# Kernel optimization log

Measured on AMD Instinct MI355X. Metric: run time of the kernel, lower is better.

The kernel has to match this reference:

```python
import jax, jax.numpy as jnp
import numpy as np

B, L = 4, 2048
D_MODEL = 64          # d_model = input_size
ED = 128              # d_inner = expand_factor * d_model = hidden_size
N = 32                # d_state
DCONV = 16            # d_conv
NLAYERS = 4
DTRANK = 4            # ceil(d_model/16)
NCLS = 1
EPS = 1e-5


def setup_inputs() -> dict:
    key = jax.random.key(0)
    ks = jax.random.split(key, 10)
    g = lambda k, s, sc: jax.random.normal(k, s, dtype=jnp.float32) * sc
    inp = {}
    inp["x"] = jax.random.normal(ks[0], (B, L, D_MODEL), dtype=jnp.float32)
    inp["in_w"] = g(ks[1], (NLAYERS, 2 * ED, D_MODEL), 0.1)
    inp["in_b"] = jnp.zeros((NLAYERS, 2 * ED), jnp.float32)
    inp["conv_w"] = g(ks[2], (NLAYERS, ED, 1, DCONV), 0.1)  # depthwise kernel (OIH per group)
    inp["conv_b"] = jnp.zeros((NLAYERS, ED), jnp.float32)
    inp["xproj_w"] = g(ks[3], (NLAYERS, DTRANK + 2 * N, ED), 0.1)
    inp["dtproj_w"] = g(ks[4], (NLAYERS, ED, DTRANK), 0.5)
    inp["dtproj_b"] = g(ks[5], (NLAYERS, ED), 0.5)
    # S4D-real init: A[e, n] = n+1
    A = jnp.tile(jnp.arange(1, N + 1, dtype=jnp.float32), (ED, 1))
    inp["A_log"] = jnp.tile(jnp.log(A)[None], (NLAYERS, 1, 1))
    inp["Dp"] = jnp.ones((NLAYERS, ED), jnp.float32)
    inp["outproj_w"] = g(ks[6], (NLAYERS, D_MODEL, ED), 0.1)
    inp["outproj_b"] = jnp.zeros((NLAYERS, D_MODEL), jnp.float32)
    inp["norm_w"] = jnp.ones((NLAYERS, D_MODEL), jnp.float32)
    inp["fc_w"] = g(ks[7], (NCLS, ED), 0.1)
    inp["fc_b"] = jnp.zeros((NCLS,), jnp.float32)
    return inp


def _rmsnorm(x, w):
    return x * jax.lax.rsqrt(jnp.mean(x * x, axis=-1, keepdims=True) + EPS) * w


def _causal_dwconv(x, w, b):
    # x: [B,L,ED], w: [ED,1,DCONV] depthwise, causal left pad
    xt = jnp.swapaxes(x, 1, 2)  # [B,ED,L]
    y = jax.lax.conv_general_dilated(
        xt, w, window_strides=(1,), padding=[(DCONV - 1, 0)],
        dimension_numbers=("NCH", "OIH", "NCH"), feature_group_count=ED)
    return jnp.swapaxes(y, 1, 2) + b


def _mamba_block(h, in_w, in_b, conv_w, conv_b, xproj_w, dtproj_w, dtproj_b,
                 A_log, Dp, outproj_w, outproj_b, last):
    xz = jnp.einsum("bld,ed->ble", h, in_w) + in_b          # [B,L,2ED]
    xin, z = jnp.split(xz, 2, axis=-1)
    xc = jax.nn.silu(_causal_dwconv(xin, conv_w, conv_b))    # [B,L,ED]
    dbc = jnp.einsum("ble,re->blr", xc, xproj_w)             # [B,L,DTRANK+2N]
    delta = dbc[..., :DTRANK]
    Bm = dbc[..., DTRANK:DTRANK + N]                          # [B,L,N]
    Cm = dbc[..., DTRANK + N:]                                # [B,L,N]
    delta = jax.nn.softplus(jnp.einsum("blr,er->ble", delta, dtproj_w) + dtproj_b)
    A = -jnp.exp(A_log)                                       # [ED,N]
    dA = jnp.exp(delta[..., None] * A)                        # [B,L,ED,N]
    dBu = delta[..., None] * Bm[:, :, None, :] * xc[..., None]  # [B,L,ED,N]

    def step(hs, t):
        dA_t, dBu_t, C_t = t                                  # [B,ED,N],[B,ED,N],[B,N]
        hs = dA_t * hs + dBu_t
        y = jnp.einsum("ben,bn->be", hs, C_t)
        return hs, y

    h0 = jnp.zeros((xc.shape[0], ED, N), dtype=xc.dtype)
    _, ys = jax.lax.scan(step, h0, (jnp.swapaxes(dA, 0, 1),
                                    jnp.swapaxes(dBu, 0, 1),
                                    jnp.swapaxes(Cm, 0, 1)))
    y = jnp.swapaxes(ys, 0, 1) + Dp * xc                      # [B,L,ED]
    y = y * jax.nn.silu(z)
    if last:
        return y                                              # classifier taps d_inner features
    return jnp.einsum("ble,de->bld", y, outproj_w) + outproj_b


def reference(x, in_w, in_b, conv_w, conv_b, xproj_w, dtproj_w, dtproj_b,
              A_log, Dp, outproj_w, outproj_b, norm_w, fc_w, fc_b):
    h = x
    for i in range(NLAYERS - 1):
        h = h + _mamba_block(_rmsnorm(h, norm_w[i]), in_w[i], in_b[i], conv_w[i],
                             conv_b[i], xproj_w[i], dtproj_w[i], dtproj_b[i],
                             A_log[i], Dp[i], outproj_w[i], outproj_b[i], False)
    i = NLAYERS - 1
    y = _mamba_block(_rmsnorm(h, norm_w[i]), in_w[i], in_b[i], conv_w[i],
                     conv_b[i], xproj_w[i], dtproj_w[i], dtproj_b[i],
                     A_log[i], Dp[i], outproj_w[i], outproj_b[i], True)
    last_hidden = y[:, -1, :]                                 # [B,ED]
    return last_hidden @ fc_w.T + fc_b                        # [B,NCLS]
```

## Files before the change

kernel.cpp:

```cpp
#include <hip/hip_runtime.h>
#include <math.h>

#define BSZ 4
#define Lseq 2048
#define DM 64
#define ED 128
#define NST 32
#define DCONVK 16
#define NLAYERS 4
#define DTRANK 4
#define EPSV 1e-5f
#define NC 128
#define TT 16
#define NSEG 8
#define GRIDN (BSZ * NC)
#define L2E 1.4426950408889634f

#if defined(__has_builtin)
#if __has_builtin(__builtin_amdgcn_exp2f)
#define EXP2F(x) __builtin_amdgcn_exp2f(x)
#else
#define EXP2F(x) exp2f(x)
#endif
#else
#define EXP2F(x) exp2f(x)
#endif

__device__ __forceinline__ float sigf(float x) { return 1.0f / (1.0f + __expf(-x)); }
__device__ __forceinline__ float hsum4(float4 a) { return (a.x + a.y) + (a.z + a.w); }

__device__ __forceinline__ float ldsc(const float* p) {
    return __hip_atomic_load((float*)p, __ATOMIC_RELAXED, __HIP_MEMORY_SCOPE_AGENT);
}
__device__ __forceinline__ void stsc(float* p, float v) {
    __hip_atomic_store(p, v, __ATOMIC_RELAXED, __HIP_MEMORY_SCOPE_AGENT);
}
__device__ __forceinline__ unsigned long long ldsc64(const void* p) {
    return __hip_atomic_load((unsigned long long*)p, __ATOMIC_RELAXED,
                             __HIP_MEMORY_SCOPE_AGENT);
}
__device__ __forceinline__ void stsc64(void* p, unsigned long long v) {
    __hip_atomic_store((unsigned long long*)p, v, __ATOMIC_RELAXED,
                       __HIP_MEMORY_SCOPE_AGENT);
}

__device__ __forceinline__ void gbar(unsigned int* cnt, unsigned int* rel,
                                     unsigned int k)
{
    __syncthreads();
    if (blockIdx.x == 0) {
        if (threadIdx.x == 0) {
            __hip_atomic_fetch_add(cnt, 1u, __ATOMIC_RELAXED, __HIP_MEMORY_SCOPE_AGENT);
            while (__hip_atomic_load(cnt, __ATOMIC_RELAXED, __HIP_MEMORY_SCOPE_AGENT)
                   < k * (unsigned)GRIDN)
                __builtin_amdgcn_s_sleep(1);
        }
        __syncthreads();
        __hip_atomic_store(&rel[threadIdx.x * 16], k,
                           __ATOMIC_RELAXED, __HIP_MEMORY_SCOPE_AGENT);
        __hip_atomic_store(&rel[(threadIdx.x + 256) * 16], k,
                           __ATOMIC_RELAXED, __HIP_MEMORY_SCOPE_AGENT);
    } else {
        if (threadIdx.x == 0) {
            __hip_atomic_fetch_add(cnt, 1u, __ATOMIC_RELAXED, __HIP_MEMORY_SCOPE_AGENT);
            while (__hip_atomic_load(&rel[blockIdx.x * 16], __ATOMIC_RELAXED,
                                     __HIP_MEMORY_SCOPE_AGENT) < k)
                __builtin_amdgcn_s_sleep(2);
        }
    }
    __builtin_amdgcn_sched_barrier(0);
    __syncthreads();
}

__device__ __forceinline__ void inproj16(
    const float* in_w_l, const float* in_b_l, const float (*hn)[DM],
    float* xin, float* zbuf, size_t t0, int tid)
{
    float4 w4[16];
    const float4* wr = (const float4*)(in_w_l + tid * DM);
    #pragma unroll
    for (int i = 0; i < 16; ++i) w4[i] = wr[i];
    const float bias = in_b_l[tid];
    #pragma unroll 2
    for (int tok = 0; tok < TT; ++tok) {
        const float4* hv4 = (const float4*)&hn[tok][0];
        float4 a4 = make_float4(0.f, 0.f, 0.f, 0.f);
        #pragma unroll
        for (int i = 0; i < 16; ++i) {
            float4 hv = hv4[i];
            a4.x = fmaf(hv.x, w4[i].x, a4.x);
            a4.y = fmaf(hv.y, w4[i].y, a4.y);
            a4.z = fmaf(hv.z, w4[i].z, a4.z);
            a4.w = fmaf(hv.w, w4[i].w, a4.w);
        }
        const float r = bias + hsum4(a4);
        if (tid < ED) stsc(&xin[(t0 + tok) * ED + tid], r);
        else          stsc(&zbuf[(t0 + tok) * ED + (tid - ED)], r);
    }
}

struct KParams {
    const float *x, *in_w, *in_b, *conv_w, *conv_b, *xproj_w, *dtproj_w,
                *dtproj_b, *A_log, *Dp, *outproj_w, *outproj_b, *norm_w,
                *fc_w, *fc_b;
    float *out, *h0, *h1, *xin, *zbuf, *xc, *dlt, *Bv, *Cv, *dsum, *hloc;
    unsigned int *cnt, *rel;
};

__global__ __launch_bounds__(256, 2) void k_mamba(KParams P)
{
    const int bid = blockIdx.x;
    const int tid = threadIdx.x;
    unsigned int bk = 0;
    __shared__ __align__(16) float smem[12288];

    if (bid == 0 && tid < BSZ) stsc(&P.out[tid], 0.f);

    {
        float (*hn)[DM] = (float (*)[DM])smem;
        const size_t t0 = (size_t)bid * TT;
        const int lane = tid & 63, wv = tid >> 6;
        const float nw = P.norm_w[lane];
        float hval[4];
        #pragma unroll
        for (int j = 0; j < 4; ++j)
            hval[j] = P.x[(t0 + wv * 4 + j) * DM + lane];
        #pragma unroll
        for (int j = 0; j < 4; ++j) {
            float ss = hval[j] * hval[j];
            #pragma unroll
            for (int off = 32; off; off >>= 1) ss += __shfl_xor(ss, off, 64);
            const float sc = rsqrtf(ss * (1.0f / DM) + EPSV);
            hn[wv * 4 + j][lane] = hval[j] * sc * nw;
        }
        __syncthreads();
        inproj16(P.in_w, P.in_b, (const float (*)[DM])hn, P.xin, P.zbuf, t0, tid);
    }
    gbar(P.cnt, P.rel, ++bk);

    #pragma unroll 1
    for (int li = 0; li < NLAYERS; ++li) {
        const int last = (li == NLAYERS - 1);
        const float* Alog = P.A_log + (size_t)li * ED * NST;
        const float* Dpl  = P.Dp + (size_t)li * ED;

        {
            const int b = bid >> 7, c = bid & 127;
            const int l0 = c * TT;
            const size_t t0 = (size_t)b * Lseq + l0;
            const int e = tid & 127, half = tid >> 7;
            const int store_dbc = last ? 0 : 1;
            const bool doXC = store_dbc || (c == NC - 1);

            float* xs = smem;
            float (*xcs)[ED] = (float (*)[ED])(smem + 4096);
            float (*Bs)[NST] = (float (*)[NST])(smem + 6144);
            float (*dts)[DTRANK] = (float (*)[DTRANK])(smem + 6656);
            float* hsT = smem + 6720;
            float (*dl)[ED] = (float (*)[ED])xs;

            const float* conv_w   = P.conv_w + (size_t)li * ED * DCONVK;
            const float* conv_b   = P.conv_b + (size_t)li * ED;
            const float* xproj_w  = P.xproj_w + (size_t)li * (DTRANK + 2 * NST) * ED;
            const float* dtproj_w = P.dtproj_w + (size_t)li * ED * DTRANK;
            const float* dtproj_b = P.dtproj_b + (size_t)li * ED;

            float Aen16[16];
            {
                const float4* a4 = (const float4*)(Alog + e * NST + half * 16);
                #pragma unroll
                for (int i = 0; i < 4; ++i) {
                    float4 v = a4[i];
                    Aen16[i*4+0] = -__expf(v.x) * L2E; Aen16[i*4+1] = -__expf(v.y) * L2E;
                    Aen16[i*4+2] = -__expf(v.z) * L2E; Aen16[i*4+3] = -__expf(v.w) * L2E;
                }
            }
            float w[DCONVK];
            {
                const float4* cw = (const float4*)(conv_w + e * DCONVK);
                #pragma unroll
                for (int i = 0; i < 4; ++i) {
                    float4 cc = cw[i];
                    w[i*4+0] = cc.x; w[i*4+1] = cc.y; w[i*4+2] = cc.z; w[i*4+3] = cc.w;
                }
            }
            const float cb = conv_b[e];

            {
                float hv[8];
                #pragma unroll
                for (int i = 0; i < 8; ++i) {
                    const int idx = tid + i * 256;
                    float val = 0.f;
                    if (idx < (DCONVK - 1) * ED) {
                        const int row = idx >> 7;
                        const int col = idx & 127;
                        const int lrow = l0 - (DCONVK - 1) + row;
                        if (lrow >= 0)
                            val = ldsc(P.xin + ((size_t)b * Lseq + lrow) * ED + col);
                    }
                    hv[i] = val;
                }
                float4 ov[2];
                #pragma unroll
                for (int i = 0; i < 2; ++i) {
                    const int idx4 = 480 + tid + i * 256;
                    const int row = idx4 >> 5;
                    const int lrow = l0 - (DCONVK - 1) + row;
                    ov[i] = ((const float4*)(P.xin + ((size_t)b * Lseq + lrow) * ED))[idx4 & 31];
                }
                #pragma unroll
                for (int i = 0; i < 8; ++i) {
                    const int idx = tid + i * 256;
                    if (idx < (DCONVK - 1) * ED) xs[idx] = hv[i];
                }
                #pragma unroll
                for (int i = 0; i < 2; ++i)
                    ((float4*)xs)[480 + tid + i * 256] = ov[i];
            }
            __syncthreads();

            {
                #pragma unroll 2
                for (int j = 0; j < 8; ++j) {
                    const int tok = half * 8 + j;
                    float acc = cb;
                    #pragma unroll
                    for (int k = 0; k < DCONVK; ++k)
                        acc = fmaf(xs[(tok + k) * ED + e], w[k], acc);
                    const float xcv = acc * sigf(acc);
                    xcs[tok][e] = xcv;
                    if (doXC) {
                        if (store_dbc) P.xc[(t0 + tok) * ED + e] = xcv;
                        else           stsc(&P.xc[(t0 + tok) * ED + e], xcv);
                    }
                }
            }
            __syncthreads();

            {
                const int wv = tid >> 6, lane = tid & 63;
                float4 acc[4];
                #pragma unroll
                for (int j = 0; j < 4; ++j) acc[j] = make_float4(0.f, 0.f, 0.f, 0.f);
                #pragma unroll 1
                for (int p = 0; p < 4; ++p) {
                    float4 w4[8];
                    const float4* wr = (const float4*)(xproj_w + lane * ED + p * 32);
                    #pragma unroll
                    for (int i = 0; i < 8; ++i) w4[i] = wr[i];
                    #pragma unroll
                    for (int j = 0; j < 4; ++j) {
                        const float4* yv = (const float4*)&xcs[wv * 4 + j][p * 32];
                        #pragma unroll
                        for (int i = 0; i < 8; ++i) {
                            float4 hv = yv[i];
                            acc[j].x = fmaf(hv.x, w4[i].x, acc[j].x);
                            acc[j].y = fmaf(hv.y, w4[i].y, acc[j].y);
                            acc[j].z = fmaf(hv.z, w4[i].z, acc[j].z);
                            acc[j].w = fmaf(hv.w, w4[i].w, acc[j].w);
                        }
                    }
                }
                #pragma unroll
                for (int j = 0; j < 4; ++j) {
                    const int tok = wv * 4 + j;
                    const float v = hsum4(acc[j]);
                    if (lane < DTRANK) {
                        dts[tok][lane] = v;
                    } else if (lane < DTRANK + NST) {
                        Bs[tok][lane - DTRANK] = v;
                        if (store_dbc) P.Bv[(t0 + tok) * NST + (lane - DTRANK)] = v;
                    } else {
                        if (doXC) {
                            const int ci = lane - DTRANK - NST;
                            if (store_dbc) P.Cv[(t0 + tok) * NST + ci] = v;
                            else           stsc(&P.Cv[(t0 + tok) * NST + ci], v);
                        }
                    }
                }
                {
                    const int ridx = lane & 3;
                    const int ks   = (lane >> 2) & 3;
                    const int tsub = lane >> 4;
                    const int r4   = 64 + ridx;
                    const int tok  = wv * 4 + tsub;
                    const float4* wr = (const float4*)(xproj_w + r4 * ED + ks * 32);
                    const float4* yv = (const float4*)&xcs[tok][ks * 32];
                    float4 a4 = make_float4(0.f, 0.f, 0.f, 0.f);
                    #pragma unroll
                    for (int i = 0; i < 8; ++i) {
                        float4 hv = yv[i]; float4 wv4 = wr[i];
                        a4.x = fmaf(hv.x, wv4.x, a4.x);
                        a4.y = fmaf(hv.y, wv4.y, a4.y);
                        a4.z = fmaf(hv.z, wv4.z, a4.z);
                        a4.w = fmaf(hv.w, wv4.w, a4.w);
                    }
                    float v = hsum4(a4);
                    v += __shfl_xor(v, 4, 64);
                    v += __shfl_xor(v, 8, 64);
                    if (ks == 0 && doXC) {
                        const int ci = r4 - DTRANK - NST;
                        if (store_dbc) P.Cv[(t0 + tok) * NST + ci] = v;
                        else           stsc(&P.Cv[(t0 + tok) * NST + ci], v);
                    }
                }
            }
            __syncthreads();

            {
                const float4 dwv = *(const float4*)(dtproj_w + e * DTRANK);
                const float bias = dtproj_b[e];
                #pragma unroll 2
                for (int j = 0; j < 8; ++j) {
                    const int tok = half * 8 + j;
                    float a = bias;
                    a = fmaf(dts[tok][0], dwv.x, a);
                    a = fmaf(dts[tok][1], dwv.y, a);
                    a = fmaf(dts[tok][2], dwv.z, a);
                    a = fmaf(dts[tok][3], dwv.w, a);
                    const float sp = fmaxf(a, 0.f) + log1pf(__expf(-fabsf(a)));
                    dl[tok][e] = sp;
                    if (store_dbc) P.dlt[(t0 + tok) * ED + e] = sp;
                }
            }
            __syncthreads();

            {
                float dsum = 0.f;
                #pragma unroll 4
                for (int l = 0; l < TT; ++l) dsum += dl[l][e];
                if (half == 0) stsc(&P.dsum[((size_t)b * NC + c) * ED + e], dsum);

                #pragma unroll 1
                for (int g = 0; g < 2; ++g) {
                    const int n0 = half * 16 + g * 8;
                    float Aen[8];
                    #pragma unroll
                    for (int k = 0; k < 8; ++k) Aen[k] = Aen16[g * 8 + k];
                    float hs[8];
                    #pragma unroll
                    for (int k = 0; k < 8; ++k) hs[k] = 0.f;
                    #pragma unroll 2
                    for (int l = 0; l < TT; ++l) {
                        const float de   = dl[l][e];
                        const float dexc = de * xcs[l][e];
                        const float4 B0 = *(const float4*)&Bs[l][n0];
                        const float4 B1 = *(const float4*)&Bs[l][n0 + 4];
                        float a;
                        a = EXP2F(de * Aen[0]); hs[0] = fmaf(a, hs[0], B0.x * dexc);
                        a = EXP2F(de * Aen[1]); hs[1] = fmaf(a, hs[1], B0.y * dexc);
                        a = EXP2F(de * Aen[2]); hs[2] = fmaf(a, hs[2], B0.z * dexc);
                        a = EXP2F(de * Aen[3]); hs[3] = fmaf(a, hs[3], B0.w * dexc);
                        a = EXP2F(de * Aen[4]); hs[4] = fmaf(a, hs[4], B1.x * dexc);
                        a = EXP2F(de * Aen[5]); hs[5] = fmaf(a, hs[5], B1.y * dexc);
                        a = EXP2F(de * Aen[6]); hs[6] = fmaf(a, hs[6], B1.z * dexc);
                        a = EXP2F(de * Aen[7]); hs[7] = fmaf(a, hs[7], B1.w * dexc);
                    }
                    #pragma unroll
                    for (int k = 0; k < 8; ++k) hsT[e * 33 + n0 + k] = hs[k];
                }
                __syncthreads();
                {
                    unsigned long long* dst =
                        (unsigned long long*)(P.hloc + (size_t)bid * (ED * NST));
                    #pragma unroll
                    for (int it = 0; it < 8; ++it) {
                        const int idx = tid + it * 256;
                        const int ee = idx >> 4;
                        const int nn = (idx & 15) * 2;
                        union { float f[2]; unsigned long long u; } pk;
                        pk.f[0] = hsT[ee * 33 + nn];
                        pk.f[1] = hsT[ee * 33 + nn + 1];
                        stsc64(dst + idx, pk.u);
                    }
                }
            }
        }
        gbar(P.cnt, P.rel, ++bk);

        {
            const int tt  = tid & 31;
            const int seg = tid >> 5;
            const int t   = bid * 32 + tt;
            const int b   = t >> 12;
            const int en  = t & 4095;
            const int e   = en >> 5;

            const float Aen2 = -__expf(Alog[en]) * L2E;

            const int c0 = seg * (NC / NSEG);
            const size_t idxBase = (size_t)b * NC * (ED * NST) + en;
            const size_t dBase   = (size_t)b * NC * ED + e;

            float u[NC / NSEG], a[NC / NSEG];
            #pragma unroll
            for (int k = 0; k < NC / NSEG; ++k)
                u[k] = ldsc(P.hloc + idxBase + (size_t)(c0 + k) * (ED * NST));
            #pragma unroll
            for (int k = 0; k < NC / NSEG; ++k)
                a[k] = EXP2F(Aen2 * ldsc(P.dsum + dBase + (size_t)(c0 + k) * ED));

            float A = 1.f, U = 0.f;
            #pragma unroll
            for (int k = 0; k < NC / NSEG; ++k) { U = fmaf(a[k], U, u[k]); A *= a[k]; }

            float (*As)[32] = (float (*)[32])smem;
            float (*Us)[32] = (float (*)[32])(smem + NSEG * 32);
            As[seg][tt] = A; Us[seg][tt] = U;
            __syncthreads();

            float h = 0.f;
            #pragma unroll
            for (int j = 0; j < NSEG - 1; ++j)
                if (j < seg) h = fmaf(As[j][tt], h, Us[j][tt]);

            #pragma unroll
            for (int k = 0; k < NC / NSEG; ++k) {
                stsc(P.hloc + idxBase + (size_t)(c0 + k) * (ED * NST), h);
                h = fmaf(a[k], h, u[k]);
            }

            if (last && seg == NSEG - 1) {
                const int n = en & 31;
                const size_t tok = (size_t)b * Lseq + (Lseq - 1);
                float p = h * ldsc(P.Cv + tok * NST + n);
                #pragma unroll
                for (int off = 16; off; off >>= 1) p += __shfl_xor(p, off, 32);
                if (n == 0) {
                    const float xce = ldsc(P.xc + tok * ED + e);
                    const float zi  = ldsc(P.zbuf + tok * ED + e);
                    float val = (p + Dpl[e] * xce) * (zi * sigf(zi)) * P.fc_w[e];
                    if (en == 0) val += P.fc_b[0];
                    atomicAdd(&P.out[b], val);
                }
            }
        }

        if (!last) {
            gbar(P.cnt, P.rel, ++bk);
            {
                const int b = bid >> 7, c = bid & 127;
                const int l0 = c * TT;
                const size_t t0 = (size_t)b * Lseq + l0;
                const int e = tid & 127, half = tid >> 7;

                float (*dlS)[ED] = (float (*)[ED])(smem);
                float (*xcS)[ED] = (float (*)[ED])(smem + 2048);
                float (*BsS)[NST] = (float (*)[NST])(smem + 4096);
                float (*CsS)[NST] = (float (*)[NST])(smem + 4608);
                float (*ys)[ED]  = (float (*)[ED])(smem + 5120);
                float (*pp)[TT][ED] = (float (*)[TT][ED])(smem + 7168);
                float (*hn)[DM]  = (float (*)[DM])(smem + 11264);

                const float* ow = P.outproj_w + (size_t)li * DM * ED;
                const float* ob = P.outproj_b + (size_t)li * DM;
                const float* hres = (li == 0) ? P.x : ((li == 1) ? P.h0 : P.h1);
                float* hout = (li & 1) ? P.h1 : P.h0;

                float Aen16[16];
                {
                    const float4* a4 = (const float4*)(Alog + e * NST + half * 16);
                    #pragma unroll
                    for (int i = 0; i < 4; ++i) {
                        float4 v = a4[i];
                        Aen16[i*4+0] = -__expf(v.x) * L2E; Aen16[i*4+1] = -__expf(v.y) * L2E;
                        Aen16[i*4+2] = -__expf(v.z) * L2E; Aen16[i*4+3] = -__expf(v.w) * L2E;
                    }
                }

                {
                    const float4* dsrc = (const float4*)(P.dlt + t0 * ED);
                    const float4* xsrc = (const float4*)(P.xc + t0 * ED);
                    float4* ddst = (float4*)&dlS[0][0];
                    float4* xdst = (float4*)&xcS[0][0];
                    #pragma unroll
                    for (int i = 0; i < 2; ++i) {
                        ddst[tid + i * 256] = dsrc[tid + i * 256];
                        xdst[tid + i * 256] = xsrc[tid + i * 256];
                    }
                    if (tid < 128) {
                        ((float4*)&BsS[0][0])[tid] = ((const float4*)(P.Bv + t0 * NST))[tid];
                        ((float4*)&CsS[0][0])[tid] = ((const float4*)(P.Cv + t0 * NST))[tid];
                    }
                }
                __syncthreads();

                #pragma unroll 1
                for (int g = 0; g < 2; ++g) {
                    const int n0 = half * 16 + g * 8;
                    float Aen[8];
                    #pragma unroll
                    for (int k = 0; k < 8; ++k) Aen[k] = Aen16[g * 8 + k];
                    float hs[8];
                    {
                        const size_t idx = (((size_t)b * NC + c) * ED + e) * NST + n0;
                        const unsigned long long* src =
                            (const unsigned long long*)(P.hloc + idx);
                        #pragma unroll
                        for (int k = 0; k < 4; ++k) {
                            union { float f[2]; unsigned long long u; } pk;
                            pk.u = ldsc64(src + k);
                            hs[2 * k]     = pk.f[0];
                            hs[2 * k + 1] = pk.f[1];
                        }
                    }
                    #pragma unroll 2
                    for (int l = 0; l < TT; ++l) {
                        const float de   = dlS[l][e];
                        const float dexc = de * xcS[l][e];
                        const float4 B0 = *(const float4*)&BsS[l][n0];
                        const float4 B1 = *(const float4*)&BsS[l][n0 + 4];
                        const float4 C0 = *(const float4*)&CsS[l][n0];
                        const float4 C1 = *(const float4*)&CsS[l][n0 + 4];
                        float a, p = 0.f;
                        a = EXP2F(de * Aen[0]); hs[0] = fmaf(a, hs[0], B0.x * dexc); p = fmaf(hs[0], C0.x, p);
                        a = EXP2F(de * Aen[1]); hs[1] = fmaf(a, hs[1], B0.y * dexc); p = fmaf(hs[1], C0.y, p);
                        a = EXP2F(de * Aen[2]); hs[2] = fmaf(a, hs[2], B0.z * dexc); p = fmaf(hs[2], C0.z, p);
                        a = EXP2F(de * Aen[3]); hs[3] = fmaf(a, hs[3], B0.w * dexc); p = fmaf(hs[3], C0.w, p);
                        a = EXP2F(de * Aen[4]); hs[4] = fmaf(a, hs[4], B1.x * dexc); p = fmaf(hs[4], C1.x, p);
                        a = EXP2F(de * Aen[5]); hs[5] = fmaf(a, hs[5], B1.y * dexc); p = fmaf(hs[5], C1.y, p);
                        a = EXP2F(de * Aen[6]); hs[6] = fmaf(a, hs[6], B1.z * dexc); p = fmaf(hs[6], C1.z, p);
                        a = EXP2F(de * Aen[7]); hs[7] = fmaf(a, hs[7], B1.w * dexc); p = fmaf(hs[7], C1.w, p);
                        if (g == 0) pp[half][l][e] = p;
                        else        pp[half][l][e] += p;
                    }
                }
                __syncthreads();
                {
                    const float dpe = Dpl[e];
                    #pragma unroll 2
                    for (int j = 0; j < 8; ++j) {
                        const int tl = half * 8 + j;
                        const size_t tok = t0 + tl;
                        const float p = pp[0][tl][e] + pp[1][tl][e];
                        const float zi = P.zbuf[tok * ED + e];
                        ys[tl][e] = (p + dpe * xcS[tl][e]) * (zi * sigf(zi));
                    }
                }
                __syncthreads();

                const int lane = tid & 63;
                const int wv = tid >> 6;
                const float nw = P.norm_w[(size_t)(li + 1) * DM + lane];
                float hval[4];
                {
                    float4 acc[4];
                    #pragma unroll
                    for (int j = 0; j < 4; ++j) acc[j] = make_float4(0.f, 0.f, 0.f, 0.f);
                    #pragma unroll 1
                    for (int p = 0; p < 4; ++p) {
                        float4 w4[8];
                        const float4* wr = (const float4*)(ow + lane * ED + p * 32);
                        #pragma unroll
                        for (int q = 0; q < 8; ++q) w4[q] = wr[q];
                        #pragma unroll
                        for (int j = 0; j < 4; ++j) {
                            const float4* yv = (const float4*)&ys[wv * 4 + j][p * 32];
                            #pragma unroll
                            for (int q = 0; q < 8; ++q) {
                                float4 hv = yv[q];
                                acc[j].x = fmaf(hv.x, w4[q].x, acc[j].x);
                                acc[j].y = fmaf(hv.y, w4[q].y, acc[j].y);
                                acc[j].z = fmaf(hv.z, w4[q].z, acc[j].z);
                                acc[j].w = fmaf(hv.w, w4[q].w, acc[j].w);
                            }
                        }
                    }
                    const float obd = ob[lane];
                    #pragma unroll
                    for (int j = 0; j < 4; ++j) {
                        const size_t tok = t0 + wv * 4 + j;
                        hval[j] = hsum4(acc[j]) + obd + hres[tok * DM + lane];
                        hout[tok * DM + lane] = hval[j];
                    }
                }
                #pragma unroll
                for (int j = 0; j < 4; ++j) {
                    float ss = hval[j] * hval[j];
                    #pragma unroll
                    for (int off = 32; off; off >>= 1) ss += __shfl_xor(ss, off, 64);
                    const float sc = rsqrtf(ss * (1.0f / DM) + EPSV);
                    hn[wv * 4 + j][lane] = hval[j] * sc * nw;
                }
                __syncthreads();
                inproj16(P.in_w + (size_t)(li + 1) * 2 * ED * DM,
                         P.in_b + (size_t)(li + 1) * 2 * ED,
                         (const float (*)[DM])hn, P.xin, P.zbuf, t0, tid);
            }
            gbar(P.cnt, P.rel, ++bk);
        }
    }
}

extern "C" void kernel_launch(void* const* d_in, const int* in_sizes, int n_in,
                              void* d_out, int out_size, void* d_ws, size_t ws_size,
                              hipStream_t stream)
{
    const size_t TOK = (size_t)BSZ * Lseq;
    float* ws = (float*)d_ws;
    float* h0    = ws; ws += TOK * DM;
    float* h1    = ws; ws += TOK * DM;
    float* xin   = ws; ws += TOK * ED;
    float* zbuf  = ws; ws += TOK * ED;
    float* xc    = ws; ws += TOK * ED;
    float* dlt   = ws; ws += TOK * ED;
    float* Bv    = ws; ws += TOK * NST;
    float* Cv    = ws; ws += TOK * NST;
    float* dsum  = ws; ws += (size_t)BSZ * NC * ED;
    float* hloc  = ws; ws += (size_t)BSZ * NC * ED * NST;
    unsigned int* cnt = (unsigned int*)ws;
    unsigned int* rel = cnt + 64;

    KParams prm;
    prm.x         = (const float*)d_in[0];
    prm.in_w      = (const float*)d_in[1];
    prm.in_b      = (const float*)d_in[2];
    prm.conv_w    = (const float*)d_in[3];
    prm.conv_b    = (const float*)d_in[4];
    prm.xproj_w   = (const float*)d_in[5];
    prm.dtproj_w  = (const float*)d_in[6];
    prm.dtproj_b  = (const float*)d_in[7];
    prm.A_log     = (const float*)d_in[8];
    prm.Dp        = (const float*)d_in[9];
    prm.outproj_w = (const float*)d_in[10];
    prm.outproj_b = (const float*)d_in[11];
    prm.norm_w    = (const float*)d_in[12];
    prm.fc_w      = (const float*)d_in[13];
    prm.fc_b      = (const float*)d_in[14];
    prm.out  = (float*)d_out;
    prm.h0 = h0; prm.h1 = h1; prm.xin = xin; prm.zbuf = zbuf;
    prm.xc = xc; prm.dlt = dlt; prm.Bv = Bv; prm.Cv = Cv;
    prm.dsum = dsum; prm.hloc = hloc; prm.cnt = cnt; prm.rel = rel;

    hipMemsetAsync(cnt, 0, (64 + 512 * 16) * sizeof(unsigned int), stream);
    k_mamba<<<dim3(GRIDN), dim3(256), 0, stream>>>(prm);
}
```

Measured before the change: 379.8 us.

## Shard grid barrier counter, add conv halo buffer, hoist hloc loads

The single global barrier counter becomes eight counters spaced 64 words apart, and block 0 polls all eight, which reduces atomic contention on one address. In-projection now writes xin and zbuf with plain stores. It separately publishes a per-block halo of the last 15 xin rows with coherent stores, and the final-token z values go to a small zbH buffer. The conv reads its halo from the previous block's halo slot and the classifier reads z from zbH, which avoids scattered coherent loads. The hloc state loads are hoisted before the dlt/xc loads. The cost is extra workspace and extra halo stores.

```diff
diff --git a/kernel.cpp b/kernel.cpp
--- a/kernel.cpp
+++ b/kernel.cpp
@@ -44,15 +44,17 @@
                        __HIP_MEMORY_SCOPE_AGENT);
 }
 
-__device__ __forceinline__ void gbar(unsigned int* cnt, unsigned int* rel,
+__device__ __forceinline__ void gbar(unsigned int* cnt8, unsigned int* rel,
                                      unsigned int k)
 {
     __syncthreads();
     if (blockIdx.x == 0) {
-        if (threadIdx.x == 0) {
-            __hip_atomic_fetch_add(cnt, 1u, __ATOMIC_RELAXED, __HIP_MEMORY_SCOPE_AGENT);
-            while (__hip_atomic_load(cnt, __ATOMIC_RELAXED, __HIP_MEMORY_SCOPE_AGENT)
-                   < k * (unsigned)GRIDN)
+        if (threadIdx.x == 0)
+            __hip_atomic_fetch_add(&cnt8[0], 1u, __ATOMIC_RELAXED,
+                                   __HIP_MEMORY_SCOPE_AGENT);
+        if (threadIdx.x < 8) {
+            while (__hip_atomic_load(&cnt8[threadIdx.x * 64], __ATOMIC_RELAXED,
+                                     __HIP_MEMORY_SCOPE_AGENT) < k * 64u)
                 __builtin_amdgcn_s_sleep(1);
         }
         __syncthreads();
@@ -62,7 +64,8 @@
                            __ATOMIC_RELAXED, __HIP_MEMORY_SCOPE_AGENT);
     } else {
         if (threadIdx.x == 0) {
-            __hip_atomic_fetch_add(cnt, 1u, __ATOMIC_RELAXED, __HIP_MEMORY_SCOPE_AGENT);
+            __hip_atomic_fetch_add(&cnt8[(blockIdx.x & 7) * 64], 1u,
+                                   __ATOMIC_RELAXED, __HIP_MEMORY_SCOPE_AGENT);
             while (__hip_atomic_load(&rel[blockIdx.x * 16], __ATOMIC_RELAXED,
                                      __HIP_MEMORY_SCOPE_AGENT) < k)
                 __builtin_amdgcn_s_sleep(2);
@@ -74,7 +77,8 @@
 
 __device__ __forceinline__ void inproj16(
     const float* in_w_l, const float* in_b_l, const float (*hn)[DM],
-    float* xin, float* zbuf, size_t t0, int tid)
+    float* xin, float* zbuf, float* haloW, float* zbH_b, bool lastChunk,
+    size_t t0, int tid)
 {
     float4 w4[16];
     const float4* wr = (const float4*)(in_w_l + tid * DM);
@@ -94,8 +98,13 @@
             a4.w = fmaf(hv.w, w4[i].w, a4.w);
         }
         const float r = bias + hsum4(a4);
-        if (tid < ED) stsc(&xin[(t0 + tok) * ED + tid], r);
-        else          stsc(&zbuf[(t0 + tok) * ED + (tid - ED)], r);
+        if (tid < ED) {
+            xin[(t0 + tok) * ED + tid] = r;
+            if (tok >= 1) stsc(&haloW[(tok - 1) * ED + tid], r);
+        } else {
+            zbuf[(t0 + tok) * ED + (tid - ED)] = r;
+            if (lastChunk && tok == TT - 1) stsc(&zbH_b[tid - ED], r);
+        }
     }
 }
 
@@ -103,7 +112,8 @@
     const float *x, *in_w, *in_b, *conv_w, *conv_b, *xproj_w, *dtproj_w,
                 *dtproj_b, *A_log, *Dp, *outproj_w, *outproj_b, *norm_w,
                 *fc_w, *fc_b;
-    float *out, *h0, *h1, *xin, *zbuf, *xc, *dlt, *Bv, *Cv, *dsum, *hloc;
+    float *out, *h0, *h1, *xin, *zbuf, *xc, *dlt, *Bv, *Cv, *dsum, *hloc,
+          *H, *zbH;
     unsigned int *cnt, *rel;
 };
 
@@ -115,6 +125,10 @@
     __shared__ __align__(16) float smem[12288];
 
     if (bid == 0 && tid < BSZ) stsc(&P.out[tid], 0.f);
+
+    const bool lastChunk = (bid & 127) == (NC - 1);
+    float* haloW = P.H + (size_t)bid * ((DCONVK - 1) * ED);
+    float* zbH_b = P.zbH + (size_t)(bid >> 7) * ED;
 
     {
         float (*hn)[DM] = (float (*)[DM])smem;
@@ -134,7 +148,8 @@
             hn[wv * 4 + j][lane] = hval[j] * sc * nw;
         }
         __syncthreads();
-        inproj16(P.in_w, P.in_b, (const float (*)[DM])hn, P.xin, P.zbuf, t0, tid);
+        inproj16(P.in_w, P.in_b, (const float (*)[DM])hn, P.xin, P.zbuf,
+                 haloW, zbH_b, lastChunk, t0, tid);
     }
     gbar(P.cnt, P.rel, ++bk);
 
@@ -192,13 +207,8 @@
                 for (int i = 0; i < 8; ++i) {
                     const int idx = tid + i * 256;
                     float val = 0.f;
-                    if (idx < (DCONVK - 1) * ED) {
-                        const int row = idx >> 7;
-                        const int col = idx & 127;
-                        const int lrow = l0 - (DCONVK - 1) + row;
-                        if (lrow >= 0)
-                            val = ldsc(P.xin + ((size_t)b * Lseq + lrow) * ED + col);
-                    }
+                    if (idx < (DCONVK - 1) * ED && c > 0)
+                        val = ldsc(P.H + (size_t)(bid - 1) * ((DCONVK - 1) * ED) + idx);
                     hv[i] = val;
                 }
                 float4 ov[2];
@@ -429,7 +439,7 @@
                 for (int off = 16; off; off >>= 1) p += __shfl_xor(p, off, 32);
                 if (n == 0) {
                     const float xce = ldsc(P.xc + tok * ED + e);
-                    const float zi  = ldsc(P.zbuf + tok * ED + e);
+                    const float zi  = ldsc(P.zbH + (size_t)b * ED + e);
                     float val = (p + Dpl[e] * xce) * (zi * sigf(zi)) * P.fc_w[e];
                     if (en == 0) val += P.fc_b[0];
                     atomicAdd(&P.out[b], val);
@@ -469,6 +479,20 @@
                     }
                 }
 
+                float hs16[16];
+                {
+                    const size_t idx = (size_t)bid * (ED * NST) + e * NST + half * 16;
+                    const unsigned long long* src =
+                        (const unsigned long long*)(P.hloc + idx);
+                    #pragma unroll
+                    for (int k = 0; k < 8; ++k) {
+                        union { float f[2]; unsigned long long u; } pk;
+                        pk.u = ldsc64(src + k);
+                        hs16[2 * k]     = pk.f[0];
+                        hs16[2 * k + 1] = pk.f[1];
+                    }
+                }
+
                 {
                     const float4* dsrc = (const float4*)(P.dlt + t0 * ED);
                     const float4* xsrc = (const float4*)(P.xc + t0 * ED);
@@ -493,18 +517,8 @@
                     #pragma unroll
                     for (int k = 0; k < 8; ++k) Aen[k] = Aen16[g * 8 + k];
                     float hs[8];
-                    {
-                        const size_t idx = (((size_t)b * NC + c) * ED + e) * NST + n0;
-                        const unsigned long long* src =
-                            (const unsigned long long*)(P.hloc + idx);
-                        #pragma unroll
-                        for (int k = 0; k < 4; ++k) {
-                            union { float f[2]; unsigned long long u; } pk;
-                            pk.u = ldsc64(src + k);
-                            hs[2 * k]     = pk.f[0];
-                            hs[2 * k + 1] = pk.f[1];
-                        }
-                    }
+                    #pragma unroll
+                    for (int k = 0; k < 8; ++k) hs[k] = hs16[g * 8 + k];
                     #pragma unroll 2
                     for (int l = 0; l < TT; ++l) {
                         const float de   = dlS[l][e];
@@ -586,7 +600,8 @@
                 __syncthreads();
                 inproj16(P.in_w + (size_t)(li + 1) * 2 * ED * DM,
                          P.in_b + (size_t)(li + 1) * 2 * ED,
-                         (const float (*)[DM])hn, P.xin, P.zbuf, t0, tid);
+                         (const float (*)[DM])hn, P.xin, P.zbuf,
+                         haloW, zbH_b, lastChunk, t0, tid);
             }
             gbar(P.cnt, P.rel, ++bk);
         }
@@ -609,8 +624,10 @@
     float* Cv    = ws; ws += TOK * NST;
     float* dsum  = ws; ws += (size_t)BSZ * NC * ED;
     float* hloc  = ws; ws += (size_t)BSZ * NC * ED * NST;
+    float* H     = ws; ws += (size_t)GRIDN * (DCONVK - 1) * ED;
+    float* zbH   = ws; ws += (size_t)BSZ * ED;
     unsigned int* cnt = (unsigned int*)ws;
-    unsigned int* rel = cnt + 64;
+    unsigned int* rel = cnt + 8 * 64;
 
     KParams prm;
     prm.x         = (const float*)d_in[0];
@@ -631,8 +648,9 @@
     prm.out  = (float*)d_out;
     prm.h0 = h0; prm.h1 = h1; prm.xin = xin; prm.zbuf = zbuf;
     prm.xc = xc; prm.dlt = dlt; prm.Bv = Bv; prm.Cv = Cv;
-    prm.dsum = dsum; prm.hloc = hloc; prm.cnt = cnt; prm.rel = rel;
-
-    hipMemsetAsync(cnt, 0, (64 + 512 * 16) * sizeof(unsigned int), stream);
+    prm.dsum = dsum; prm.hloc = hloc; prm.H = H; prm.zbH = zbH;
+    prm.cnt = cnt; prm.rel = rel;
+
+    hipMemsetAsync(cnt, 0, (8 * 64 + 512 * 16) * sizeof(unsigned int), stream);
     k_mamba<<<dim3(GRIDN), dim3(256), 0, stream>>>(prm);
 }
```

Result: faster. 370.6 us (-2.4%).
